# Kernel optimization log

Measured on AMD Instinct MI355X. Metric: run time of the kernel, lower is better.

The kernel has to match this reference:

```python
import jax, jax.numpy as jnp
import numpy as np

B, S, D, H = 2, 2048, 1024, 16
DK = D // H


def setup_inputs() -> dict:
    key = jax.random.key(0)
    ks = jax.random.split(key, 12)
    scale = 1.0 / np.sqrt(D)
    inp = {
        "query": jax.random.normal(ks[0], (B, S, D), jnp.float32),
        "key": jax.random.normal(ks[1], (B, S, D), jnp.float32),
        "value": jax.random.normal(ks[2], (B, S, D), jnp.float32),
        "mask": jax.random.randint(ks[3], (B, 1, S, S), 0, 2, jnp.int32),
        "Wq": jax.random.normal(ks[4], (D, D), jnp.float32) * scale,
        "bq": jnp.zeros((D,), jnp.float32),
        "Wk": jax.random.normal(ks[5], (D, D), jnp.float32) * scale,
        "bk": jnp.zeros((D,), jnp.float32),
        "Wv": jax.random.normal(ks[6], (D, D), jnp.float32) * scale,
        "bv": jnp.zeros((D,), jnp.float32),
        "Wo": jax.random.normal(ks[7], (D, D), jnp.float32) * scale,
        "bo": jnp.zeros((D,), jnp.float32),
    }
    return inp


def reference(query, key, value, mask, Wq, bq, Wk, bk, Wv, bv, Wo, bo):
    # Linear projections (dropout is identity in eval mode)
    q = query @ Wq + bq          # (B,S,D)
    k = key @ Wk + bk
    v = value @ Wv + bv

    # split heads: (B,S,D) -> (B,H,S,DK)
    def split(x):
        return x.reshape(B, S, H, DK).transpose(0, 2, 1, 3)

    q, k, v = split(q), split(k), split(v)

    scores = jnp.einsum("bhqd,bhkd->bhqk", q, k) / jnp.sqrt(jnp.float32(DK))
    scores = jnp.where(mask == 0, jnp.float32(-1e9), scores)
    p_attn = jax.nn.softmax(scores, axis=-1)   # (B,H,S,S)

    att = jnp.einsum("bhqk,bhkd->bhqd", p_attn, v)  # (B,H,S,DK)
    merged = att.transpose(0, 2, 1, 3).reshape(B, S, D)
    return merged @ Wo + bo
```

## Files before the change

kernel.cpp:

```cpp
#include <hip/hip_runtime.h>
#include <hip/hip_bf16.h>
#include <cstdint>
#include <cstddef>


#define B_ 2
#define S_ 2048
#define D_ 1024
#define H_ 16
#define M_ 4096

typedef unsigned short u16;
typedef __attribute__((ext_vector_type(8))) short bf16x8;
typedef __attribute__((ext_vector_type(8))) unsigned short u16x8;
typedef __attribute__((ext_vector_type(4))) unsigned short u16x4;
typedef __attribute__((ext_vector_type(4))) unsigned int u32x4;
typedef __attribute__((ext_vector_type(4))) float f32x4;
typedef __attribute__((ext_vector_type(4))) int i32x4;

#define QSCALE 0.18033688011112042f

__device__ __forceinline__ u16 f2bf(float f) {
  __hip_bfloat16 h = __float2bfloat16(f);
  return *reinterpret_cast<u16*>(&h);
}

__device__ __forceinline__ unsigned cvtpk(float lo, float hi) {
  unsigned r;
  asm("v_cvt_pk_bf16_f32 %0, %1, %2" : "=v"(r) : "v"(lo), "v"(hi));
  return r;
}

__device__ __forceinline__ void gload_lds16(const void* g, void* l) {
  __builtin_amdgcn_global_load_lds((const __attribute__((address_space(1))) void*)g,
                                   (__attribute__((address_space(3))) void*)l, 16, 0, 0);
}

__global__ __launch_bounds__(256) void k_convert(const float* __restrict__ q, const float* __restrict__ k,
                                                 const float* __restrict__ v,
                                                 u16* __restrict__ xq, u16* __restrict__ xk, u16* __restrict__ xv) {
  int z = blockIdx.y;
  const float* src = (z == 0) ? q : (z == 1) ? k : v;
  u16* dst = (z == 0) ? xq : (z == 1) ? xk : xv;
  size_t i = ((size_t)blockIdx.x * 256 + threadIdx.x) * 8;
  f32x4 a = *(const f32x4*)(src + i);
  f32x4 b = *(const f32x4*)(src + i + 4);
  u16x8 o;
  o[0]=f2bf(a[0]); o[1]=f2bf(a[1]); o[2]=f2bf(a[2]); o[3]=f2bf(a[3]);
  o[4]=f2bf(b[0]); o[5]=f2bf(b[1]); o[6]=f2bf(b[2]); o[7]=f2bf(b[3]);
  *(u16x8*)(dst + i) = o;
}

__global__ __launch_bounds__(256) void k_transposeW(const float* __restrict__ w0, const float* __restrict__ w1,
                                                    const float* __restrict__ w2, const float* __restrict__ w3,
                                                    u16* __restrict__ t0, u16* __restrict__ t1,
                                                    u16* __restrict__ t2, u16* __restrict__ t3) {
  int z = blockIdx.z;
  const float* W = (z==0)?w0:(z==1)?w1:(z==2)?w2:w3;
  u16* Wt = (z==0)?t0:(z==1)?t1:(z==2)?t2:t3;
  __shared__ float tile[32][33];
  int tx = threadIdx.x & 31, ty = threadIdx.x >> 5;
  int bx = blockIdx.x * 32, by = blockIdx.y * 32;
  #pragma unroll
  for (int p = 0; p < 4; ++p)
    tile[ty + p*8][tx] = W[(size_t)(by + ty + p*8) * D_ + bx + tx];
  __syncthreads();
  #pragma unroll
  for (int p = 0; p < 4; ++p)
    Wt[(size_t)(bx + ty + p*8) * D_ + by + tx] = f2bf(tile[tx][ty + p*8]);
}

__global__ __launch_bounds__(256) void k_packmask(const int* __restrict__ mask, u16* __restrict__ out) {
  size_t t = (size_t)blockIdx.x * 256 + threadIdx.x;
  const int* p = mask + t * 64;
  unsigned wds0 = 0, wds1 = 0, wds2 = 0, wds3 = 0;
  #pragma unroll
  for (int c = 0; c < 16; ++c) {
    i32x4 v = *(const i32x4*)(p + c*4);
    #pragma unroll
    for (int e = 0; e < 4; ++e) {
      const int k = c*4 + e;
      const int lcw = (k >> 3) & 3;
      const int ni = ((k >> 4) & 2) | ((k >> 2) & 1);
      const unsigned bit = 1u << (4*ni + (k & 3));
      if (v[e]) {
        if (lcw == 0) wds0 |= bit; else if (lcw == 1) wds1 |= bit;
        else if (lcw == 2) wds2 |= bit; else wds3 |= bit;
      }
    }
  }
  u16x4 w; w[0] = (u16)wds0; w[1] = (u16)wds1; w[2] = (u16)wds2; w[3] = (u16)wds3;
  *(u16x4*)(out + t*4) = w;
}

template<int CMODE, int MI, int NI>
__device__ __forceinline__ void gemm_core(const u16* __restrict__ A, const u16* __restrict__ Bt,
                                          const float* __restrict__ bias, void* __restrict__ Cv,
                                          float scale, int bm, int bn) {
  extern __shared__ u16 sm[];
  constexpr int ASZ = MI*32*64;
  u16* As = sm;
  u16* Bs = sm + ASZ;
  const int t = threadIdx.x;
  const int l = t & 63, w = t >> 6;
  const int wr = w >> 1, wc = w & 1;
  const int lr = l & 15, lc = l >> 4;
  f32x4 acc[MI][NI];
  #pragma unroll
  for (int i = 0; i < MI; ++i)
    #pragma unroll
    for (int j = 0; j < NI; ++j) { f32x4 z = {0.f,0.f,0.f,0.f}; acc[i][j] = z; }
  const int srow = t >> 3;
  const int blkx = (t & 7) ^ (srow & 7);
  const u16* ga = A  + (size_t)(bm*(MI*32) + srow)*1024 + blkx*8;
  const u16* gb = Bt + (size_t)(bn*(NI*32) + srow)*1024 + blkx*8;
  for (int kt = 0; kt < 16; ++kt) {
    const int ko = kt * 64;
    __syncthreads();
    #pragma unroll
    for (int i = 0; i < MI; ++i)
      gload_lds16(ga + (size_t)(i*32)*1024 + ko, &As[i*2048 + t*8]);
    #pragma unroll
    for (int i = 0; i < NI; ++i)
      gload_lds16(gb + (size_t)(i*32)*1024 + ko, &Bs[i*2048 + t*8]);
    __syncthreads();
    #pragma unroll
    for (int ks = 0; ks < 2; ++ks) {
      bf16x8 af[MI], bfr[NI];
      #pragma unroll
      for (int mi = 0; mi < MI; ++mi)
        af[mi]  = *(const bf16x8*)&As[(wr*(MI*16) + mi*16 + lr)*64 + (((ks*4 + lc) ^ (lr & 7))*8)];
      #pragma unroll
      for (int ni = 0; ni < NI; ++ni)
        bfr[ni] = *(const bf16x8*)&Bs[(wc*(NI*16) + ni*16 + lr)*64 + (((ks*4 + lc) ^ (lr & 7))*8)];
      #pragma unroll
      for (int mi = 0; mi < MI; ++mi)
        #pragma unroll
        for (int ni = 0; ni < NI; ++ni)
          acc[mi][ni] = __builtin_amdgcn_mfma_f32_16x16x32_bf16(af[mi], bfr[ni], acc[mi][ni], 0, 0, 0);
    }
  }
  #pragma unroll
  for (int ni = 0; ni < NI; ++ni) {
    int gcol = bn*(NI*32) + wc*(NI*16) + ni*16 + lr;
    float bv = bias[gcol];
    #pragma unroll
    for (int mi = 0; mi < MI; ++mi) {
      int grow = bm*(MI*32) + wr*(MI*16) + mi*16 + lc*4;
      if (CMODE == 2) {
        u16x4 pk;
        #pragma unroll
        for (int j = 0; j < 4; ++j) pk[j] = f2bf((acc[mi][ni][j] + bv) * scale);
        *(u16x4*)&((u16*)Cv)[(size_t)gcol * M_ + grow] = pk;
      } else {
        #pragma unroll
        for (int j = 0; j < 4; ++j) {
          float v = (acc[mi][ni][j] + bv) * scale;
          if (CMODE == 0) ((u16*)Cv)[(size_t)(grow + j) * 1024 + gcol] = f2bf(v);
          else            ((float*)Cv)[(size_t)(grow + j) * 1024 + gcol] = v;
        }
      }
    }
  }
}

__global__ __launch_bounds__(256, 4) void k_gemm_qkv(const u16* Xq, const u16* Xk, const u16* Xv,
                                                     const u16* Wqt, const u16* Wkt, const u16* Wvt,
                                                     const float* bq, const float* bk, const float* bv,
                                                     u16* Qo, u16* Ko, u16* Vt, float qscale) {
  const int id = blockIdx.x + (blockIdx.y << 5) + (blockIdx.z << 8);
  const int lg = (id & 7) * 96 + (id >> 3);
  const int bm = lg & 31;
  const int panel = lg >> 5;
  const int bn = panel & 7, z = panel >> 3;
  if (z == 0)      gemm_core<0,4,4>(Xq, Wqt, bq, Qo, qscale, bm, bn);
  else if (z == 1) gemm_core<0,4,4>(Xk, Wkt, bk, Ko, 1.f,    bm, bn);
  else             gemm_core<2,4,4>(Xv, Wvt, bv, Vt, 1.f,    bm, bn);
}

__global__ __launch_bounds__(256, 4) void k_gemm_out(const u16* Aatt, const u16* Wot, const float* bo, float* out) {
  const int id = blockIdx.x + (blockIdx.y << 5);
  const int lg = (id & 7) * 64 + (id >> 3);
  const int bm = lg & 31, bn = lg >> 5;
  gemm_core<1,4,2>(Aatt, Wot, bo, out, 1.f, bm, bn);
}

__global__ __launch_bounds__(512, 4) void k_attn(const u16* __restrict__ Q, const u16* __restrict__ Kb,
                                                 const u16* __restrict__ Vt,
                                                 const u16* __restrict__ mbw,
                                                 u16* __restrict__ attb) {
  __shared__ u16 Ks[3*4096];
  __shared__ u16 Vs[2*4096];
  const int t = threadIdx.x, l = t & 63, w = t >> 6;
  const int lr = l & 15, lc = l >> 4;
  const int id = blockIdx.x + (blockIdx.y << 4) + (blockIdx.z << 8);
  const int lg = (id & 7) * 64 + (id >> 3);
  const int qt = lg & 15, h = (lg >> 4) & 15, b = lg >> 8;
  const int r0 = t >> 3;
  const int c0 = (t & 7) ^ (r0 & 7);
  const int pr0 = (r0 & 32) | ((r0 & 12) << 1) | ((r0 & 16) >> 2) | (r0 & 3);
  const u16* kp0 = Kb + (size_t)(b*S_ + pr0)*D_ + h*64 + c0*8;
  const u16* vp0 = Vt + (size_t)(h*64 + r0)*M_ + b*S_ + c0*8;

  gload_lds16(Q + (size_t)(b*S_ + qt*128 + r0)*D_      + h*64 + c0*8, &Ks[t*8]);
  gload_lds16(Q + (size_t)(b*S_ + qt*128 + 64 + r0)*D_ + h*64 + c0*8, &Ks[4096 + t*8]);
  __syncthreads();
  const int qrow = w*16 + lr;
  const int sw0 = ((lc     ) ^ (lr & 7)) * 8;
  const int sw1 = ((4 + lc ) ^ (lr & 7)) * 8;
  const int qbuf = (qrow >> 6) * 4096, qrl = (qrow & 63) * 64;
  bf16x8 aq0 = *(const bf16x8*)&Ks[qbuf + qrl + sw0];
  bf16x8 aq1 = *(const bf16x8*)&Ks[qbuf + qrl + sw1];
  __syncthreads();
  gload_lds16(kp0,                  &Ks[t*8]);
  gload_lds16(vp0,                  &Vs[t*8]);
  gload_lds16(kp0 + (size_t)64*D_,  &Ks[4096 + t*8]);

  const short one_bf = (short)0x3F80;
  const bf16x8 onesf = {one_bf,one_bf,one_bf,one_bf,one_bf,one_bf,one_bf,one_bf};
  f32x4 ls = {0.f,0.f,0.f,0.f};
  f32x4 o[4];
  #pragma unroll
  for (int ni = 0; ni < 4; ++ni) { f32x4 z = {0.f,0.f,0.f,0.f}; o[ni] = z; }
  const u16* mkp = mbw + (size_t)(b*S_ + qt*128 + qrow)*128 + lc;
  const u16* vpA = vp0;
  const u16* kpA = kp0;

#define AITER(N, KC, VC, VN, KNN, KPRE, VPRE, WAITN) {                                 \
    asm volatile("s_waitcnt vmcnt(" #WAITN ")");                                       \
    __builtin_amdgcn_s_barrier();                                                      \
    __builtin_amdgcn_sched_barrier(0);                                                 \
    unsigned mw = mkp[(N)*4];                                                          \
    if (VPRE) gload_lds16(vpA + ((N)+1)*64,              &Vs[(VN)*4096 + t*8]);        \
    if (KPRE) gload_lds16(kpA + (size_t)((N)+2)*64*D_,   &Ks[(KNN)*4096 + t*8]);       \
    f32x4 s[4];                                                                        \
    _Pragma("unroll")                                                                  \
    for (int ni = 0; ni < 4; ++ni) { f32x4 z = {0.f,0.f,0.f,0.f}; s[ni] = z; }         \
    __builtin_amdgcn_s_setprio(1);                                                     \
    _Pragma("unroll")                                                                  \
    for (int ni = 0; ni < 4; ++ni) {                                                   \
      bf16x8 bk0 = *(const bf16x8*)&Ks[(KC)*4096 + (ni*16 + lr)*64 + sw0];             \
      bf16x8 bk1 = *(const bf16x8*)&Ks[(KC)*4096 + (ni*16 + lr)*64 + sw1];             \
      s[ni] = __builtin_amdgcn_mfma_f32_16x16x32_bf16(bk0, aq0, s[ni], 0, 0, 0);       \
      s[ni] = __builtin_amdgcn_mfma_f32_16x16x32_bf16(bk1, aq1, s[ni], 0, 0, 0);       \
    }                                                                                  \
    __builtin_amdgcn_s_setprio(0);                                                     \
    _Pragma("unroll")                                                                  \
    for (int ni = 0; ni < 4; ++ni)                                                     \
      _Pragma("unroll")                                                                \
      for (int j = 0; j < 4; ++j) {                                                    \
        float pv = __builtin_amdgcn_exp2f(s[ni][j]);                                   \
        int bmsk = ((int)(mw << (31 - (4*ni + j)))) >> 31;                             \
        union { float f; int i; } u; u.f = pv; u.i &= bmsk;                            \
        s[ni][j] = u.f;                                                                \
      }                                                                                \
    u32x4 pw0, pw1;                                                                    \
    pw0[0] = cvtpk(s[0][0], s[0][1]); pw0[1] = cvtpk(s[0][2], s[0][3]);                \
    pw0[2] = cvtpk(s[1][0], s[1][1]); pw0[3] = cvtpk(s[1][2], s[1][3]);                \
    pw1[0] = cvtpk(s[2][0], s[2][1]); pw1[1] = cvtpk(s[2][2], s[2][3]);                \
    pw1[2] = cvtpk(s[3][0], s[3][1]); pw1[3] = cvtpk(s[3][2], s[3][3]);                \
    bf16x8 pa0 = __builtin_bit_cast(bf16x8, pw0);                                      \
    bf16x8 pa1 = __builtin_bit_cast(bf16x8, pw1);                                      \
    __builtin_amdgcn_s_setprio(1);                                                     \
    ls = __builtin_amdgcn_mfma_f32_16x16x32_bf16(pa0, onesf, ls, 0, 0, 0);             \
    ls = __builtin_amdgcn_mfma_f32_16x16x32_bf16(pa1, onesf, ls, 0, 0, 0);             \
    _Pragma("unroll")                                                                  \
    for (int ni = 0; ni < 4; ++ni) {                                                   \
      bf16x8 bv0 = *(const bf16x8*)&Vs[(VC)*4096 + (ni*16 + lr)*64 + sw0];             \
      o[ni] = __builtin_amdgcn_mfma_f32_16x16x32_bf16(pa0, bv0, o[ni], 0, 0, 0);       \
    }                                                                                  \
    _Pragma("unroll")                                                                  \
    for (int ni = 0; ni < 4; ++ni) {                                                   \
      bf16x8 bv1 = *(const bf16x8*)&Vs[(VC)*4096 + (ni*16 + lr)*64 + sw1];             \
      o[ni] = __builtin_amdgcn_mfma_f32_16x16x32_bf16(pa1, bv1, o[ni], 0, 0, 0);       \
    }                                                                                  \
    __builtin_amdgcn_s_setprio(0);                                                     \
  }

  for (int it = 0; it < 5; ++it) {
    AITER(0, 0,0, 1,2, 1,1, 1);
    AITER(1, 1,1, 0,0, 1,1, 1);
    AITER(2, 2,0, 1,1, 1,1, 1);
    AITER(3, 0,1, 0,2, 1,1, 1);
    AITER(4, 1,0, 1,0, 1,1, 1);
    AITER(5, 2,1, 0,1, 1,1, 1);
    mkp += 24;
    vpA += 6*64;
    kpA += (size_t)6*64*D_;
  }
  AITER(0, 0,0, 1,0, 0,1, 1);
  AITER(1, 1,1, 0,0, 0,0, 0);
#undef AITER

  float rl[4];
  #pragma unroll
  for (int j = 0; j < 4; ++j) rl[j] = 1.f / ls[j];
  #pragma unroll
  for (int ni = 0; ni < 4; ++ni)
    #pragma unroll
    for (int j = 0; j < 4; ++j) {
      int orow = qt*128 + w*16 + lc*4 + j, dcol = ni*16 + lr;
      attb[(size_t)(b*S_ + orow)*D_ + h*64 + dcol] = f2bf(o[ni][j] * rl[j]);
    }
}

extern "C" void kernel_launch(void* const* d_in, const int* in_sizes, int n_in,
                              void* d_out, int out_size, void* d_ws, size_t ws_size,
                              hipStream_t stream) {
  (void)in_sizes; (void)n_in; (void)out_size; (void)ws_size;
  const float* query = (const float*)d_in[0];
  const float* key   = (const float*)d_in[1];
  const float* value = (const float*)d_in[2];
  const int*   mask  = (const int*)d_in[3];
  const float* Wq = (const float*)d_in[4];
  const float* bq = (const float*)d_in[5];
  const float* Wk = (const float*)d_in[6];
  const float* bk = (const float*)d_in[7];
  const float* Wv = (const float*)d_in[8];
  const float* bv = (const float*)d_in[9];
  const float* Wo = (const float*)d_in[10];
  const float* bo = (const float*)d_in[11];
  float* out = (float*)d_out;
  char* ws = (char*)d_ws;
  const size_t MB = 1024 * 1024;
  u16* Xq  = (u16*)(ws + 0*MB);
  u16* Xk  = (u16*)(ws + 8*MB);
  u16* Xv  = (u16*)(ws + 16*MB);
  u16* Wqt = (u16*)(ws + 24*MB);
  u16* Wkt = (u16*)(ws + 26*MB);
  u16* Wvt = (u16*)(ws + 28*MB);
  u16* Wot = (u16*)(ws + 30*MB);
  u16* Qb  = (u16*)(ws + 32*MB);
  u16* Kb  = (u16*)(ws + 40*MB);
  u16* Vtb = (u16*)(ws + 48*MB);
  u16* mbits = (u16*)(ws + 56*MB);
  u16* attb = (u16*)(ws + 0*MB);

  k_convert  <<<dim3(2048, 3),     256, 0,     stream>>>(query, key, value, Xq, Xk, Xv);
  k_transposeW<<<dim3(32, 32, 4),  256, 0,     stream>>>(Wq, Wk, Wv, Wo, Wqt, Wkt, Wvt, Wot);
  k_packmask <<<dim3(512),         256, 0,     stream>>>(mask, mbits);
  k_gemm_qkv <<<dim3(32, 8, 3),    256, 32768, stream>>>(Xq, Xk, Xv, Wqt, Wkt, Wvt, bq, bk, bv,
                                                         Qb, Kb, Vtb, QSCALE);
  k_attn     <<<dim3(16, 16, 2),   512, 0,     stream>>>(Qb, Kb, Vtb, mbits, attb);
  k_gemm_out <<<dim3(32, 16),      256, 24576, stream>>>(attb, Wot, bo, out);
}
```

Measured before the change: 131.7 us.

## Software-pipeline attention loop: overlap QK^T of next tile with softmax-PV of previous

Restructures the attention inner loop so each phase computes QK^T scores for tile N while doing exp/mask/PV for tile N-1, using two score register sets. The V buffer grows to triple buffering to support the one-tile skew, with a prologue and epilogue added. The intent is to give the scheduler independent MFMA work to hide exp and LDS latency. In exchange it raises register pressure and LDS usage, which could reduce occupancy under the 512x4 launch bounds.

```diff
diff --git a/kernel.cpp b/kernel.cpp
--- a/kernel.cpp
+++ b/kernel.cpp
@@ -190,7 +190,7 @@
                                                  const u16* __restrict__ mbw,
                                                  u16* __restrict__ attb) {
   __shared__ u16 Ks[3*4096];
-  __shared__ u16 Vs[2*4096];
+  __shared__ u16 Vs[3*4096];
   const int t = threadIdx.x, l = t & 63, w = t >> 6;
   const int lr = l & 15, lc = l >> 4;
   const int id = blockIdx.x + (blockIdx.y << 4) + (blockIdx.z << 8);
@@ -220,45 +220,38 @@
   const bf16x8 onesf = {one_bf,one_bf,one_bf,one_bf,one_bf,one_bf,one_bf,one_bf};
   f32x4 ls = {0.f,0.f,0.f,0.f};
   f32x4 o[4];
+  f32x4 s_a[4], s_b[4];
   #pragma unroll
   for (int ni = 0; ni < 4; ++ni) { f32x4 z = {0.f,0.f,0.f,0.f}; o[ni] = z; }
-  const u16* mkp = mbw + (size_t)(b*S_ + qt*128 + qrow)*128 + lc;
-  const u16* vpA = vp0;
-  const u16* kpA = kp0;
-
-#define AITER(N, KC, VC, VN, KNN, KPRE, VPRE, WAITN) {                                 \
-    asm volatile("s_waitcnt vmcnt(" #WAITN ")");                                       \
-    __builtin_amdgcn_s_barrier();                                                      \
-    __builtin_amdgcn_sched_barrier(0);                                                 \
-    unsigned mw = mkp[(N)*4];                                                          \
-    if (VPRE) gload_lds16(vpA + ((N)+1)*64,              &Vs[(VN)*4096 + t*8]);        \
-    if (KPRE) gload_lds16(kpA + (size_t)((N)+2)*64*D_,   &Ks[(KNN)*4096 + t*8]);       \
-    f32x4 s[4];                                                                        \
-    _Pragma("unroll")                                                                  \
-    for (int ni = 0; ni < 4; ++ni) { f32x4 z = {0.f,0.f,0.f,0.f}; s[ni] = z; }         \
+
+#define QKP(SC, KC) {                                                                  \
+    _Pragma("unroll")                                                                  \
+    for (int ni = 0; ni < 4; ++ni) { f32x4 z = {0.f,0.f,0.f,0.f}; SC[ni] = z; }        \
     __builtin_amdgcn_s_setprio(1);                                                     \
     _Pragma("unroll")                                                                  \
     for (int ni = 0; ni < 4; ++ni) {                                                   \
       bf16x8 bk0 = *(const bf16x8*)&Ks[(KC)*4096 + (ni*16 + lr)*64 + sw0];             \
       bf16x8 bk1 = *(const bf16x8*)&Ks[(KC)*4096 + (ni*16 + lr)*64 + sw1];             \
-      s[ni] = __builtin_amdgcn_mfma_f32_16x16x32_bf16(bk0, aq0, s[ni], 0, 0, 0);       \
-      s[ni] = __builtin_amdgcn_mfma_f32_16x16x32_bf16(bk1, aq1, s[ni], 0, 0, 0);       \
+      SC[ni] = __builtin_amdgcn_mfma_f32_16x16x32_bf16(bk0, aq0, SC[ni], 0, 0, 0);     \
+      SC[ni] = __builtin_amdgcn_mfma_f32_16x16x32_bf16(bk1, aq1, SC[ni], 0, 0, 0);     \
     }                                                                                  \
     __builtin_amdgcn_s_setprio(0);                                                     \
+  }
+
+#define SMPV(SP, MW, VCP) {                                                            \
     _Pragma("unroll")                                                                  \
     for (int ni = 0; ni < 4; ++ni)                                                     \
       _Pragma("unroll")                                                                \
       for (int j = 0; j < 4; ++j) {                                                    \
-        float pv = __builtin_amdgcn_exp2f(s[ni][j]);                                   \
-        int bmsk = ((int)(mw << (31 - (4*ni + j)))) >> 31;                             \
-        union { float f; int i; } u; u.f = pv; u.i &= bmsk;                            \
-        s[ni][j] = u.f;                                                                \
+        float pv = __builtin_amdgcn_exp2f(SP[ni][j]);                                  \
+        int bmsk = ((int)((MW) << (31 - (4*ni + j)))) >> 31;                           \
+        union { float f; int i; } uu; uu.f = pv; uu.i &= bmsk; SP[ni][j] = uu.f;       \
       }                                                                                \
     u32x4 pw0, pw1;                                                                    \
-    pw0[0] = cvtpk(s[0][0], s[0][1]); pw0[1] = cvtpk(s[0][2], s[0][3]);                \
-    pw0[2] = cvtpk(s[1][0], s[1][1]); pw0[3] = cvtpk(s[1][2], s[1][3]);                \
-    pw1[0] = cvtpk(s[2][0], s[2][1]); pw1[1] = cvtpk(s[2][2], s[2][3]);                \
-    pw1[2] = cvtpk(s[3][0], s[3][1]); pw1[3] = cvtpk(s[3][2], s[3][3]);                \
+    pw0[0] = cvtpk(SP[0][0], SP[0][1]); pw0[1] = cvtpk(SP[0][2], SP[0][3]);            \
+    pw0[2] = cvtpk(SP[1][0], SP[1][1]); pw0[3] = cvtpk(SP[1][2], SP[1][3]);            \
+    pw1[0] = cvtpk(SP[2][0], SP[2][1]); pw1[1] = cvtpk(SP[2][2], SP[2][3]);            \
+    pw1[2] = cvtpk(SP[3][0], SP[3][1]); pw1[3] = cvtpk(SP[3][2], SP[3][3]);            \
     bf16x8 pa0 = __builtin_bit_cast(bf16x8, pw0);                                      \
     bf16x8 pa1 = __builtin_bit_cast(bf16x8, pw1);                                      \
     __builtin_amdgcn_s_setprio(1);                                                     \
@@ -266,31 +259,68 @@
     ls = __builtin_amdgcn_mfma_f32_16x16x32_bf16(pa1, onesf, ls, 0, 0, 0);             \
     _Pragma("unroll")                                                                  \
     for (int ni = 0; ni < 4; ++ni) {                                                   \
-      bf16x8 bv0 = *(const bf16x8*)&Vs[(VC)*4096 + (ni*16 + lr)*64 + sw0];             \
+      bf16x8 bv0 = *(const bf16x8*)&Vs[(VCP)*4096 + (ni*16 + lr)*64 + sw0];            \
       o[ni] = __builtin_amdgcn_mfma_f32_16x16x32_bf16(pa0, bv0, o[ni], 0, 0, 0);       \
     }                                                                                  \
     _Pragma("unroll")                                                                  \
     for (int ni = 0; ni < 4; ++ni) {                                                   \
-      bf16x8 bv1 = *(const bf16x8*)&Vs[(VC)*4096 + (ni*16 + lr)*64 + sw1];             \
+      bf16x8 bv1 = *(const bf16x8*)&Vs[(VCP)*4096 + (ni*16 + lr)*64 + sw1];            \
       o[ni] = __builtin_amdgcn_mfma_f32_16x16x32_bf16(pa1, bv1, o[ni], 0, 0, 0);       \
     }                                                                                  \
     __builtin_amdgcn_s_setprio(0);                                                     \
   }
 
+#define PH(N, KC, VCP, VN, KNN, SCUR, SPREV) {                                         \
+    asm volatile("s_waitcnt vmcnt(2)");                                                \
+    __builtin_amdgcn_s_barrier();                                                      \
+    __builtin_amdgcn_sched_barrier(0);                                                 \
+    unsigned mw = mkp[(N)*4];                                                          \
+    gload_lds16(vpA + ((N)+1)*64,            &Vs[(VN)*4096 + t*8]);                    \
+    gload_lds16(kpA + (size_t)((N)+2)*64*D_, &Ks[(KNN)*4096 + t*8]);                   \
+    QKP(SCUR, KC);                                                                     \
+    SMPV(SPREV, mw, VCP);                                                              \
+  }
+
+  asm volatile("s_waitcnt vmcnt(2)");
+  __builtin_amdgcn_s_barrier();
+  __builtin_amdgcn_sched_barrier(0);
+  gload_lds16(vp0 + 64,                &Vs[4096 + t*8]);
+  gload_lds16(kp0 + (size_t)2*64*D_,   &Ks[2*4096 + t*8]);
+  QKP(s_a, 0);
+
+  const u16* mkp = mbw + (size_t)(b*S_ + qt*128 + qrow)*128 + lc;
+  const u16* vpA = vp0 + 64;
+  const u16* kpA = kp0 + (size_t)64*D_;
+
   for (int it = 0; it < 5; ++it) {
-    AITER(0, 0,0, 1,2, 1,1, 1);
-    AITER(1, 1,1, 0,0, 1,1, 1);
-    AITER(2, 2,0, 1,1, 1,1, 1);
-    AITER(3, 0,1, 0,2, 1,1, 1);
-    AITER(4, 1,0, 1,0, 1,1, 1);
-    AITER(5, 2,1, 0,1, 1,1, 1);
+    PH(0, 1, 0, 2, 0, s_b, s_a);
+    PH(1, 2, 1, 0, 1, s_a, s_b);
+    PH(2, 0, 2, 1, 2, s_b, s_a);
+    PH(3, 1, 0, 2, 0, s_a, s_b);
+    PH(4, 2, 1, 0, 1, s_b, s_a);
+    PH(5, 0, 2, 1, 2, s_a, s_b);
     mkp += 24;
     vpA += 6*64;
     kpA += (size_t)6*64*D_;
   }
-  AITER(0, 0,0, 1,0, 0,1, 1);
-  AITER(1, 1,1, 0,0, 0,0, 0);
-#undef AITER
+  {
+    asm volatile("s_waitcnt vmcnt(2)");
+    __builtin_amdgcn_s_barrier();
+    __builtin_amdgcn_sched_barrier(0);
+    unsigned mw = mkp[0];
+    QKP(s_b, 1);
+    SMPV(s_a, mw, 0);
+  }
+  {
+    asm volatile("s_waitcnt vmcnt(1)");
+    __builtin_amdgcn_s_barrier();
+    __builtin_amdgcn_sched_barrier(0);
+    unsigned mw = mkp[4];
+    SMPV(s_b, mw, 1);
+  }
+#undef PH
+#undef SMPV
+#undef QKP
 
   float rl[4];
   #pragma unroll
```

Measured after the change: 132.2 us. About the same (+0.4%).
